# Kernel optimization log

Hardware: AMD Instinct MI355X
Metric: run time of the kernel (lower is better)

Reference implementation:

```python
import jax, jax.numpy as jnp
import numpy as np

H, D, K = 8, 64, 9           # new num heads, head size, conv kernel size
A = H * D                    # all_head_size = 512
HID = 2 * A                  # input hidden size = 1024
STD = 0.02


def setup_inputs() -> dict:
    key = jax.random.key(0)
    ks = jax.random.split(key, 16)
    B, S = 4, 2048
    f = jnp.float32
    inp = {
        'hidden_states': jax.random.normal(ks[0], (B, S, HID), f),
        'Wq': jax.random.normal(ks[1], (A, A), f) * STD,
        'bq': jnp.zeros((A,), f),
        'Wk': jax.random.normal(ks[2], (A, A), f) * STD,
        'bk': jnp.zeros((A,), f),
        'Wv': jax.random.normal(ks[3], (A, A), f) * STD,
        'bv': jnp.zeros((A,), f),
        'dw_w': jax.random.normal(ks[4], (A, 1, K), f) * STD,   # depthwise conv (groups=A)
        'pw_w': jax.random.normal(ks[5], (A, A, 1), f) * STD,   # pointwise 1x1 conv
        'sep_b': jnp.zeros((A, 1), f),                          # SeparableConv1D bias
        'Wck': jax.random.normal(ks[6], (H * K, A), f) * STD,   # conv_kernel_layer
        'bck': jnp.zeros((H * K,), f),
        'Wco': jax.random.normal(ks[7], (A, A), f) * STD,       # conv_out_layer
        'bco': jnp.zeros((A,), f),
    }
    return inp


def reference(hidden_states, Wq, bq, Wk, bk, Wv, bv, dw_w, pw_w, sep_b, Wck, bck, Wco, bco):
    B, S, _ = hidden_states.shape
    hs_attn = hidden_states[:, :, :A]
    hs_conv = hidden_states[:, :, A:]

    q = hs_attn @ Wq.T + bq
    k = hs_attn @ Wk.T + bk
    v = hs_attn @ Wv.T + bv

    # SeparableConv1D on (B, A, S): depthwise then pointwise, plus bias
    x = hs_conv.transpose(0, 2, 1)
    x = jax.lax.conv_general_dilated(
        x, dw_w, window_strides=(1,), padding=[(K // 2, K // 2)],
        feature_group_count=A, dimension_numbers=('NCH', 'OIH', 'NCH'))
    x = jnp.einsum('bcs,oc->bos', x, pw_w[:, :, 0]) + sep_b
    mixed_key_conv = x.transpose(0, 2, 1)            # (B,S,A)

    # per-token softmax conv kernel
    conv_attn = mixed_key_conv * hs_conv
    ckl = (conv_attn @ Wck.T + bck).reshape(B, S, H, K)
    ckl = jax.nn.softmax(ckl, axis=-1)               # softmax over kernel taps

    # dynamic-span lightweight convolution (unfold -> batched matmul)
    col = hs_conv @ Wco.T + bco                      # (B,S,A)
    pad = jnp.pad(col, ((0, 0), (K // 2, K // 2), (0, 0)))
    windows = jnp.stack([pad[:, i:i + S] for i in range(K)], axis=-1)  # (B,S,A,K)
    windows = windows.reshape(B, S, H, D, K)
    conv_out = jnp.einsum('bshdk,bshk->bshd', windows, ckl)            # (B,S,H,D)

    # standard self-attention
    qh = q.reshape(B, S, H, D).transpose(0, 2, 1, 3)
    kh = k.reshape(B, S, H, D).transpose(0, 2, 1, 3)
    vh = v.reshape(B, S, H, D).transpose(0, 2, 1, 3)
    scale = jnp.asarray(1.0 / np.sqrt(D), q.dtype)
    scores = jnp.einsum('bhqd,bhkd->bhqk', qh, kh) * scale
    probs = jax.nn.softmax(scores, axis=-1)
    ctx = jnp.einsum('bhqk,bhkd->bqhd', probs, vh)   # (B,S,H,D)

    out = jnp.concatenate([ctx, conv_out], axis=2)   # (B,S,2H,D)
    return out.reshape(B, S, HID)
```

## Files before the change

kernel.cpp:

```cpp
#include <hip/hip_runtime.h>
#include <hip/hip_bf16.h>

#define NH   8
#define HD   64
#define KW   9
#define AD   512
#define HIDD 1024
#define BB   4
#define SS   2048
#define MTOK (BB*SS)
#define WSZ  262144

typedef __attribute__((ext_vector_type(8))) short short8;
typedef __attribute__((ext_vector_type(4))) float floatx4;
typedef __attribute__((ext_vector_type(16))) float floatx16;

__device__ __forceinline__ short f2bf(float f) {
    unsigned u = __float_as_uint(f);
    u = (u + 0x7FFFu + ((u >> 16) & 1u)) >> 16;
    return (short)u;
}
__device__ __forceinline__ float bf2f(short s) {
    return __uint_as_float(((unsigned)(unsigned short)s) << 16);
}
__device__ __forceinline__ float exp2_raw(float x) {
    return __builtin_amdgcn_exp2f(x);
}
__device__ __forceinline__ unsigned pkbf2(float a, float b) {
    unsigned au = __float_as_uint(a) + 0x8000u;
    unsigned bu = __float_as_uint(b) + 0x8000u;
    return __builtin_amdgcn_perm(bu, au, 0x07060302);
}
__device__ __forceinline__ void gl2lds16(const short* g, short* l) {
    __builtin_amdgcn_global_load_lds(
        (const __attribute__((address_space(1))) void*)g,
        (__attribute__((address_space(3))) void*)l, 16, 0, 0);
}

__global__ __launch_bounds__(256) void cvt_hs_kernel(
    const float* __restrict__ hs, short* __restrict__ hsb)
{
    int idx = blockIdx.x * 256 + threadIdx.x;
    const float* s = hs + (long)idx * 8;
    float4 a = *(const float4*)s, c = *(const float4*)(s + 4);
    short8 o;
    o[0]=f2bf(a.x); o[1]=f2bf(a.y); o[2]=f2bf(a.z); o[3]=f2bf(a.w);
    o[4]=f2bf(c.x); o[5]=f2bf(c.y); o[6]=f2bf(c.z); o[7]=f2bf(c.w);
    *(short8*)(hsb + (long)idx * 8) = o;
}

__global__ __launch_bounds__(256) void cvt_w_kernel(
    const float* __restrict__ pw, const float* __restrict__ Wco,
    const float* __restrict__ Wq, const float* __restrict__ Wk,
    const float* __restrict__ Wv, const float* __restrict__ Wck,
    const float* __restrict__ dw,
    short* __restrict__ dst, float* __restrict__ dwT)
{
    int idx = blockIdx.x * 256 + threadIdx.x;
    if (idx >= 172032) {
        int t = idx - 172032;
        if (t < AD * KW) {
            int c = t / KW, k = t - c * KW;
            dwT[k * AD + c] = dw[t];
        }
        return;
    }
    int e0 = idx * 8;
    short8 o;
    if (e0 < 5 * WSZ) {
        int w = e0 >> 18, off = e0 & (WSZ - 1);
        const float* src = (w == 0) ? pw : (w == 1) ? Wco : (w == 2) ? Wq
                         : (w == 3) ? Wk : Wv;
        float4 a = *(const float4*)(src + off), c = *(const float4*)(src + off + 4);
        o[0]=f2bf(a.x); o[1]=f2bf(a.y); o[2]=f2bf(a.z); o[3]=f2bf(a.w);
        o[4]=f2bf(c.x); o[5]=f2bf(c.y); o[6]=f2bf(c.z); o[7]=f2bf(c.w);
    } else {
        int off = e0 - 5 * WSZ;
        int row = off >> 9, col = off & 511;
        if (row < NH * KW) {
            const float* src = Wck + row * AD + col;
            float4 a = *(const float4*)src, c = *(const float4*)(src + 4);
            o[0]=f2bf(a.x); o[1]=f2bf(a.y); o[2]=f2bf(a.z); o[3]=f2bf(a.w);
            o[4]=f2bf(c.x); o[5]=f2bf(c.y); o[6]=f2bf(c.z); o[7]=f2bf(c.w);
        } else {
            for (int i = 0; i < 8; ++i) o[i] = 0;
        }
    }
    *(short8*)(dst + e0) = o;
}

__global__ __launch_bounds__(256) void dwconv_kernel(
    const short* __restrict__ hsb, const float* __restrict__ dwT,
    short* __restrict__ x1)
{
    int idx = blockIdx.x * 256 + threadIdx.x;
    int c8  = (idx & 63) * 8;
    int tok = idx >> 6;
    int s   = tok & (SS - 1);
    int b   = tok >> 11;
    const short* base = hsb + (long)(b * SS) * HIDD + AD + c8;
    float acc[8];
#pragma unroll
    for (int i = 0; i < 8; ++i) acc[i] = 0.f;
#pragma unroll
    for (int kk = 0; kk < KW; ++kk) {
        int ss2 = s + kk - KW / 2;
        if (ss2 >= 0 && ss2 < SS) {
            short8 hv = *(const short8*)(base + (long)ss2 * HIDD);
            float4 w0 = *(const float4*)(dwT + kk * AD + c8);
            float4 w1 = *(const float4*)(dwT + kk * AD + c8 + 4);
            acc[0] += w0.x * bf2f(hv[0]); acc[1] += w0.y * bf2f(hv[1]);
            acc[2] += w0.z * bf2f(hv[2]); acc[3] += w0.w * bf2f(hv[3]);
            acc[4] += w1.x * bf2f(hv[4]); acc[5] += w1.y * bf2f(hv[5]);
            acc[6] += w1.z * bf2f(hv[6]); acc[7] += w1.w * bf2f(hv[7]);
        }
    }
    short8 o;
#pragma unroll
    for (int i = 0; i < 8; ++i) o[i] = f2bf(acc[i]);
    *(short8*)(x1 + (long)tok * AD + c8) = o;
}

template<int FM, int FN, int MODE>
__global__ __launch_bounds__(256) void gemm_bf16_kernel(
    const short* __restrict__ X, int ldx, int xoff,
    const short* __restrict__ W,
    const float* __restrict__ b0p, const float* __restrict__ b1p,
    const float* __restrict__ b2p,
    const short* __restrict__ mulp, int mul_ld, int mul_off,
    void* __restrict__ Cout, short* __restrict__ vtout,
    int ldc, int N, int Kd, float oscale)
{
    constexpr int TM = 32 * FM, TN = 32 * FN;
    __shared__ __align__(16) short As[TM * 64];
    __shared__ __align__(16) short Bs[TN * 64];
    const int tid  = threadIdx.x;
    const int wv   = tid >> 6, lane = tid & 63;
    const int ln   = lane & 15, quad = lane >> 4;
    const int wm   = wv >> 1, wn = wv & 1;
    const int m0 = blockIdx.x * TM, n0 = blockIdx.y * TN;

    floatx4 acc[FM][FN];
#pragma unroll
    for (int i = 0; i < FM; ++i)
#pragma unroll
        for (int j = 0; j < FN; ++j) acc[i][j] = (floatx4){0.f, 0.f, 0.f, 0.f};

    const short* xbase = X + (long)m0 * ldx + xoff;
    const short* wbase = W + (long)n0 * Kd;

    for (int k0 = 0; k0 < Kd; k0 += 64) {
#pragma unroll
        for (int g = tid; g < TM * 8; g += 256) {
            int m = g >> 3, p = g & 7, gk = p ^ (m & 7);
            gl2lds16(xbase + (long)m * ldx + k0 + gk * 8, &As[g * 8]);
        }
#pragma unroll
        for (int g = tid; g < TN * 8; g += 256) {
            int m = g >> 3, p = g & 7, gk = p ^ (m & 7);
            gl2lds16(wbase + (long)m * Kd + k0 + gk * 8, &Bs[g * 8]);
        }
        __syncthreads();
#pragma unroll
        for (int half = 0; half < 2; ++half) {
            short8 afr[FM], bfr[FN];
#pragma unroll
            for (int i = 0; i < FM; ++i) {
                int p = (half * 4 + quad) ^ (ln & 7);
                afr[i] = *(const short8*)&As[(wm * 16 * FM + i * 16 + ln) * 64 + p * 8];
            }
#pragma unroll
            for (int j = 0; j < FN; ++j) {
                int p = (half * 4 + quad) ^ (ln & 7);
                bfr[j] = *(const short8*)&Bs[(wn * 16 * FN + j * 16 + ln) * 64 + p * 8];
            }
#pragma unroll
            for (int i = 0; i < FM; ++i)
#pragma unroll
                for (int j = 0; j < FN; ++j)
                    acc[i][j] = __builtin_amdgcn_mfma_f32_16x16x32_bf16(
                        afr[i], bfr[j], acc[i][j], 0, 0, 0);
        }
        __syncthreads();
    }

#pragma unroll
    for (int j = 0; j < FN; ++j) {
        int n = n0 + wn * 16 * FN + j * 16 + ln;
        if constexpr (MODE == 3) {
            if (n >= 1024) {
                int hh = (n - 1024) >> 6, dd = (n - 1024) & 63;
                float bv = b2p[n - 1024];
                int mblk = m0 + wm * 16 * FM;
                int bidx = mblk >> 11, sblk = mblk & (SS - 1);
                short* dst = vtout + ((long)((bidx * NH + hh) * HD + dd)) * SS + sblk;
#pragma unroll
                for (int i = 0; i < FM; ++i) {
                    unsigned lo = pkbf2(acc[i][j][0] + bv, acc[i][j][1] + bv);
                    unsigned hi = pkbf2(acc[i][j][2] + bv, acc[i][j][3] + bv);
                    *(uint2*)(dst + i * 16 + quad * 4) = make_uint2(lo, hi);
                }
            } else {
                float bv = (n < 512) ? b0p[n] : b1p[n - 512];
                float sc = (n < 512) ? oscale : 1.f;
#pragma unroll
                for (int i = 0; i < FM; ++i) {
#pragma unroll
                    for (int r = 0; r < 4; ++r) {
                        int m = m0 + wm * 16 * FM + i * 16 + quad * 4 + r;
                        float val = (acc[i][j][r] + bv) * sc;
                        ((short*)Cout)[(long)m * ldc + n] = f2bf(val);
                    }
                }
            }
        } else if (n < N) {
            float bv = b0p[n], sc = oscale;
#pragma unroll
            for (int i = 0; i < FM; ++i) {
#pragma unroll
                for (int r = 0; r < 4; ++r) {
                    int m = m0 + wm * 16 * FM + i * 16 + quad * 4 + r;
                    float val = (acc[i][j][r] + bv) * sc;
                    if constexpr (MODE == 2)
                        val *= bf2f(mulp[(long)m * mul_ld + mul_off + n]);
                    if constexpr (MODE == 0)
                        ((float*)Cout)[(long)m * ldc + n] = val;
                    else
                        ((short*)Cout)[(long)m * ldc + n] = f2bf(val);
                }
            }
        }
    }
}

__global__ __launch_bounds__(256) void convout_kernel(
    const short* __restrict__ col, const float* __restrict__ ckl,
    float* __restrict__ out)
{
    int idx = blockIdx.x * 256 + threadIdx.x;
    int d4  = (idx & 127) * 4;
    int tok = idx >> 7;
    int s   = tok & (SS - 1);
    int b   = tok >> 11;
    int h   = d4 >> 6;
    const float* lg = ckl + (long)tok * (NH * KW) + h * KW;
    float wv[KW];
    float mx = -1e30f;
#pragma unroll
    for (int i = 0; i < KW; ++i) { wv[i] = lg[i]; mx = fmaxf(mx, wv[i]); }
    float sum = 0.f;
#pragma unroll
    for (int i = 0; i < KW; ++i) { wv[i] = __expf(wv[i] - mx); sum += wv[i]; }
    float inv = 1.f / sum;
    float a0 = 0.f, a1 = 0.f, a2 = 0.f, a3 = 0.f;
    const short* cbase = col + (long)(b * SS) * AD + d4;
#pragma unroll
    for (int kk = 0; kk < KW; ++kk) {
        int ss2 = s + kk - KW / 2;
        if (ss2 >= 0 && ss2 < SS) {
            uint2 cv = *(const uint2*)(cbase + (long)ss2 * AD);
            float w = wv[kk];
            a0 += w * bf2f((short)(cv.x & 0xFFFF));
            a1 += w * bf2f((short)(cv.x >> 16));
            a2 += w * bf2f((short)(cv.y & 0xFFFF));
            a3 += w * bf2f((short)(cv.y >> 16));
        }
    }
    *(float4*)&out[(long)tok * HIDD + AD + d4] =
        make_float4(a0 * inv, a1 * inv, a2 * inv, a3 * inv);
}

__global__ __launch_bounds__(256) void flash_mfma_kernel(
    const short* __restrict__ qkv, const short* __restrict__ vT,
    float* __restrict__ out)
{
    const int qt = blockIdx.x, h = blockIdx.y, b = blockIdx.z;
    const int tid  = threadIdx.x;
    const int w    = tid >> 6;
    const int lane = tid & 63;
    const int l5   = lane & 31;
    const int hh   = lane >> 5;

    __shared__ __align__(16) short Kb[64 * 64];
    __shared__ __align__(16) short Vt[64 * 64];
    __shared__ float ls[4][32];

    const int  q0 = qt * 128 + w * 32;
    const long rowbase = (long)b * SS;

    short8 qf[4];
    {
        const short* qrow = qkv + (rowbase + q0 + l5) * 1536 + h * HD;
#pragma unroll
        for (int i = 0; i < 4; ++i)
            qf[i] = *(const short8*)(qrow + i * 16 + hh * 8);
    }

    floatx16 acc0, acc1;
#pragma unroll
    for (int r = 0; r < 16; ++r) { acc0[r] = 0.f; acc1[r] = 0.f; }
    float l_i = 0.f;

    const int m1 = tid >> 3,  gk1 = (tid & 7) ^ (m1 & 7);
    const int g2 = 256 + tid;
    const int m2 = g2 >> 3,   gk2 = (g2 & 7) ^ (m2 & 7);
    const short* kbase  = qkv + 512 + rowbase * 1536 + h * HD;
    const short* vtbase = vT + ((long)(b * NH + h) * HD) * SS;
    const short* sk0 = kbase  + (long)m1 * 1536 + gk1 * 8;
    const short* sk1 = kbase  + (long)m2 * 1536 + gk2 * 8;
    const short* sv0 = vtbase + (long)m1 * SS   + gk1 * 8;
    const short* sv1 = vtbase + (long)m2 * SS   + gk2 * 8;
    short* const dk0 = &Kb[tid * 8];
    short* const dk1 = &Kb[g2 * 8];
    short* const dv0 = &Vt[tid * 8];
    short* const dv1 = &Vt[g2 * 8];

#define STAGE_K() do { gl2lds16(sk0, dk0); gl2lds16(sk1, dk1); \
                       sk0 += 64 * 1536; sk1 += 64 * 1536; } while (0)
#define STAGE_V() do { gl2lds16(sv0, dv0); gl2lds16(sv1, dv1); \
                       sv0 += 64; sv1 += 64; } while (0)

    auto qkt_pack = [&](short8* pf) {
        floatx16 S0, S1;
#pragma unroll
        for (int r = 0; r < 16; ++r) { S0[r] = 0.f; S1[r] = 0.f; }
#pragma unroll
        for (int i = 0; i < 4; ++i) {
            int p = (2 * i + hh) ^ (l5 & 7);
            short8 k0 = *(const short8*)&Kb[l5 * 64 + p * 8];
            short8 k1 = *(const short8*)&Kb[(32 + l5) * 64 + p * 8];
            S0 = __builtin_amdgcn_mfma_f32_32x32x16_bf16(k0, qf[i], S0, 0, 0, 0);
            S1 = __builtin_amdgcn_mfma_f32_32x32x16_bf16(k1, qf[i], S1, 0, 0, 0);
        }
        float pe0[16], pe1[16];
#pragma unroll
        for (int r = 0; r < 16; ++r) {
            pe0[r] = exp2_raw(S0[r]);
            pe1[r] = exp2_raw(S1[r]);
        }
        float s = 0.f;
#pragma unroll
        for (int r = 0; r < 16; ++r) s += pe0[r] + pe1[r];
        l_i += s;
#pragma unroll
        for (int t = 0; t < 2; ++t) {
            const float* pe = t ? pe1 : pe0;
#pragma unroll
            for (int u = 0; u < 2; ++u) {
                unsigned a0 = pkbf2(pe[8 * u + 0], pe[8 * u + 1]);
                unsigned a1 = pkbf2(pe[8 * u + 2], pe[8 * u + 3]);
                unsigned b0 = pkbf2(pe[8 * u + 4], pe[8 * u + 5]);
                unsigned b1 = pkbf2(pe[8 * u + 6], pe[8 * u + 7]);
                asm("v_permlane32_swap_b32 %0, %1" : "+v"(a0), "+v"(b0));
                asm("v_permlane32_swap_b32 %0, %1" : "+v"(a1), "+v"(b1));
                union { uint4 u4; short8 s8; } cv;
                cv.u4 = make_uint4(a0, a1, b0, b1);
                pf[t * 2 + u] = cv.s8;
            }
        }
    };

    auto pv_phase = [&](const short8* pf) {
#pragma unroll
        for (int s = 0; s < 4; ++s) {
            int p = (2 * s + hh) ^ (l5 & 7);
            short8 v0 = *(const short8*)&Vt[l5 * 64 + p * 8];
            short8 v1 = *(const short8*)&Vt[(32 + l5) * 64 + p * 8];
            acc0 = __builtin_amdgcn_mfma_f32_32x32x16_bf16(pf[s], v0, acc0, 0, 0, 0);
            acc1 = __builtin_amdgcn_mfma_f32_32x32x16_bf16(pf[s], v1, acc1, 0, 0, 0);
        }
    };

    STAGE_K();
    STAGE_V();
    asm volatile("s_waitcnt vmcnt(0)" ::: "memory");
    __builtin_amdgcn_s_barrier();
    asm volatile("" ::: "memory");

    const int NT = SS / 64;
    short8 pf[4];
    for (int kt = 0; kt < NT - 1; ++kt) {
        qkt_pack(pf);
        __builtin_amdgcn_s_barrier();
        asm volatile("" ::: "memory");
        STAGE_K();
        asm volatile("s_waitcnt vmcnt(2)" ::: "memory");
        __builtin_amdgcn_s_barrier();
        asm volatile("" ::: "memory");
        pv_phase(pf);
        __builtin_amdgcn_s_barrier();
        asm volatile("" ::: "memory");
        STAGE_V();
        asm volatile("s_waitcnt vmcnt(2)" ::: "memory");
        __builtin_amdgcn_s_barrier();
        asm volatile("" ::: "memory");
    }
    qkt_pack(pf);
    asm volatile("s_waitcnt vmcnt(0)" ::: "memory");
    __builtin_amdgcn_s_barrier();
    asm volatile("" ::: "memory");
    pv_phase(pf);

#undef STAGE_K
#undef STAGE_V

    l_i += __shfl_xor(l_i, 32);
    ls[w][l5] = 1.f / l_i;
    float4 lv[4];
#pragma unroll
    for (int g = 0; g < 4; ++g)
        lv[g] = *(const float4*)&ls[w][8 * g + 4 * hh];

#pragma unroll
    for (int r = 0; r < 16; ++r) {
        int g = r >> 2, j = r & 3;
        int qr = j + 8 * g + 4 * hh;
        float iv = lv[g][j];
        float* orow = out + (rowbase + q0 + qr) * HIDD + h * HD;
        orow[l5]      = acc0[r] * iv;
        orow[32 + l5] = acc1[r] * iv;
    }
}

extern "C" void kernel_launch(void* const* d_in, const int* in_sizes, int n_in,
                              void* d_out, int out_size, void* d_ws, size_t ws_size,
                              hipStream_t stream)
{
    const float* hs   = (const float*)d_in[0];
    const float* Wq   = (const float*)d_in[1];
    const float* bq   = (const float*)d_in[2];
    const float* Wk   = (const float*)d_in[3];
    const float* bk   = (const float*)d_in[4];
    const float* Wv   = (const float*)d_in[5];
    const float* bv   = (const float*)d_in[6];
    const float* dw   = (const float*)d_in[7];
    const float* pw   = (const float*)d_in[8];
    const float* sepb = (const float*)d_in[9];
    const float* Wck  = (const float*)d_in[10];
    const float* bck  = (const float*)d_in[11];
    const float* Wco  = (const float*)d_in[12];
    const float* bco  = (const float*)d_in[13];
    float* out = (float*)d_out;

    short* hsb  = (short*)d_ws;
    short* x1c  = hsb + (long)MTOK * HIDD;
    short* qkvb = x1c + (long)MTOK * AD;
    short* vTb  = qkvb + (long)MTOK * 1536;
    float* ckl  = (float*)(vTb + (long)MTOK * AD);
    short* wb   = (short*)(ckl + (long)MTOK * (NH * KW));
    short* pw_b   = wb;
    short* Wco_b  = wb + 1L * WSZ;
    short* Wqkv_b = wb + 2L * WSZ;
    short* Wck_b  = wb + 5L * WSZ;
    float* dwT    = (float*)(Wck_b + 128L * AD);
    short* cab    = qkvb;

    const float QSCALE = 0.18033688011112042f;

    cvt_hs_kernel<<<MTOK * HIDD / 2048, 256, 0, stream>>>(hs, hsb);
    cvt_w_kernel<<<690, 256, 0, stream>>>(
        pw, Wco, Wq, Wk, Wv, Wck, dw, wb, dwT);
    dwconv_kernel<<<MTOK * AD / 2048, 256, 0, stream>>>(hsb, dwT, x1c);
    gemm_bf16_kernel<2, 2, 2><<<dim3(MTOK / 64, AD / 64), 256, 0, stream>>>(
        x1c, AD, 0, pw_b, sepb, nullptr, nullptr, hsb, HIDD, AD,
        cab, nullptr, AD, AD, AD, 1.f);
    gemm_bf16_kernel<2, 2, 0><<<dim3(MTOK / 64, 2), 256, 0, stream>>>(
        cab, AD, 0, Wck_b, bck, nullptr, nullptr, nullptr, 0, 0,
        ckl, nullptr, NH * KW, NH * KW, AD, 1.f);
    gemm_bf16_kernel<2, 2, 1><<<dim3(MTOK / 64, AD / 64), 256, 0, stream>>>(
        hsb, HIDD, AD, Wco_b, bco, nullptr, nullptr, nullptr, 0, 0,
        x1c, nullptr, AD, AD, AD, 1.f);
    convout_kernel<<<MTOK * AD / 1024, 256, 0, stream>>>(x1c, ckl, out);
    gemm_bf16_kernel<4, 4, 3><<<dim3(MTOK / 128, 1536 / 128), 256, 0, stream>>>(
        hsb, HIDD, 0, Wqkv_b, bq, bk, bv, nullptr, 0, 0,
        qkvb, vTb, 1536, 1536, AD, QSCALE);
    flash_mfma_kernel<<<dim3(SS / 128, NH, BB), 256, 0, stream>>>(qkvb, vTb, out);

    (void)in_sizes; (void)n_in; (void)out_size; (void)ws_size;
}
```

Baseline: 232.9 us.

## Split flash attention keys across wave pairs and merge partial results in LDS

The flash attention kernel now uses 64 queries per block, with two wave pairs each handling alternate 64-key tiles. Their partial accumulators and row sums are reduced through shared memory at the end, and the grid doubles to 1024 blocks, giving more parallelism across CUs. It also packs bf16 with the hardware v_cvt_pk_bf16_f32 instruction, raises MFMA wave priority with s_setprio, and sets a launch-bounds occupancy hint. The exchange is an extra LDS reduction step, more total staging traffic for Q, and possible register pressure from the occupancy hint.

```diff
diff --git a/kernel.cpp b/kernel.cpp
--- a/kernel.cpp
+++ b/kernel.cpp
@@ -27,9 +27,9 @@
     return __builtin_amdgcn_exp2f(x);
 }
 __device__ __forceinline__ unsigned pkbf2(float a, float b) {
-    unsigned au = __float_as_uint(a) + 0x8000u;
-    unsigned bu = __float_as_uint(b) + 0x8000u;
-    return __builtin_amdgcn_perm(bu, au, 0x07060302);
+    unsigned d;
+    asm("v_cvt_pk_bf16_f32 %0, %1, %2" : "=v"(d) : "v"(a), "v"(b));
+    return d;
 }
 __device__ __forceinline__ void gl2lds16(const short* g, short* l) {
     __builtin_amdgcn_global_load_lds(
@@ -270,7 +270,7 @@
         make_float4(a0 * inv, a1 * inv, a2 * inv, a3 * inv);
 }
 
-__global__ __launch_bounds__(256) void flash_mfma_kernel(
+__global__ __launch_bounds__(256, 4) void flash_mfma_kernel(
     const short* __restrict__ qkv, const short* __restrict__ vT,
     float* __restrict__ out)
 {
@@ -280,12 +280,18 @@
     const int lane = tid & 63;
     const int l5   = lane & 31;
     const int hh   = lane >> 5;
-
-    __shared__ __align__(16) short Kb[64 * 64];
-    __shared__ __align__(16) short Vt[64 * 64];
-    __shared__ float ls[4][32];
-
-    const int  q0 = qt * 128 + w * 32;
+    const int qhalf = w & 1;
+    const int kpar  = w >> 1;
+    const int ptid  = tid & 127;
+
+    __shared__ __align__(16) short smem[4][4096];
+    __shared__ float ls[2][32];
+    float* const cbuf = (float*)smem;
+
+    short* const Kb = smem[kpar];
+    short* const Vt = smem[2 + kpar];
+
+    const int  q0 = qt * 64 + qhalf * 32;
     const long rowbase = (long)b * SS;
 
     short8 qf[4];
@@ -301,29 +307,44 @@
     for (int r = 0; r < 16; ++r) { acc0[r] = 0.f; acc1[r] = 0.f; }
     float l_i = 0.f;
 
-    const int m1 = tid >> 3,  gk1 = (tid & 7) ^ (m1 & 7);
-    const int g2 = 256 + tid;
-    const int m2 = g2 >> 3,   gk2 = (g2 & 7) ^ (m2 & 7);
-    const short* kbase  = qkv + 512 + rowbase * 1536 + h * HD;
-    const short* vtbase = vT + ((long)(b * NH + h) * HD) * SS;
-    const short* sk0 = kbase  + (long)m1 * 1536 + gk1 * 8;
-    const short* sk1 = kbase  + (long)m2 * 1536 + gk2 * 8;
-    const short* sv0 = vtbase + (long)m1 * SS   + gk1 * 8;
-    const short* sv1 = vtbase + (long)m2 * SS   + gk2 * 8;
-    short* const dk0 = &Kb[tid * 8];
-    short* const dk1 = &Kb[g2 * 8];
-    short* const dv0 = &Vt[tid * 8];
-    short* const dv1 = &Vt[g2 * 8];
-
-#define STAGE_K() do { gl2lds16(sk0, dk0); gl2lds16(sk1, dk1); \
-                       sk0 += 64 * 1536; sk1 += 64 * 1536; } while (0)
-#define STAGE_V() do { gl2lds16(sv0, dv0); gl2lds16(sv1, dv1); \
-                       sv0 += 64; sv1 += 64; } while (0)
+    const short* kb_s[4];
+    const short* vt_s[4];
+    short* kb_d[4];
+    short* vt_d[4];
+    {
+        const short* kbase  = qkv + 512 + rowbase * 1536 + h * HD
+                            + (long)kpar * 64 * 1536;
+        const short* vtbase = vT + ((long)(b * NH + h) * HD) * SS + kpar * 64;
+#pragma unroll
+        for (int j = 0; j < 4; ++j) {
+            int g = ptid + 128 * j, m = g >> 3, p = g & 7, gk = p ^ (m & 7);
+            kb_s[j] = kbase + (long)m * 1536 + gk * 8;
+            vt_s[j] = vtbase + (long)m * SS + gk * 8;
+            kb_d[j] = &Kb[g * 8];
+            vt_d[j] = &Vt[g * 8];
+        }
+    }
+
+    auto STAGE_K = [&]() {
+#pragma unroll
+        for (int j = 0; j < 4; ++j) {
+            gl2lds16(kb_s[j], kb_d[j]);
+            kb_s[j] += 128 * 1536;
+        }
+    };
+    auto STAGE_V = [&]() {
+#pragma unroll
+        for (int j = 0; j < 4; ++j) {
+            gl2lds16(vt_s[j], vt_d[j]);
+            vt_s[j] += 128;
+        }
+    };
 
     auto qkt_pack = [&](short8* pf) {
         floatx16 S0, S1;
 #pragma unroll
         for (int r = 0; r < 16; ++r) { S0[r] = 0.f; S1[r] = 0.f; }
+        __builtin_amdgcn_s_setprio(1);
 #pragma unroll
         for (int i = 0; i < 4; ++i) {
             int p = (2 * i + hh) ^ (l5 & 7);
@@ -332,6 +353,7 @@
             S0 = __builtin_amdgcn_mfma_f32_32x32x16_bf16(k0, qf[i], S0, 0, 0, 0);
             S1 = __builtin_amdgcn_mfma_f32_32x32x16_bf16(k1, qf[i], S1, 0, 0, 0);
         }
+        __builtin_amdgcn_s_setprio(0);
         float pe0[16], pe1[16];
 #pragma unroll
         for (int r = 0; r < 16; ++r) {
@@ -361,6 +383,7 @@
     };
 
     auto pv_phase = [&](const short8* pf) {
+        __builtin_amdgcn_s_setprio(1);
 #pragma unroll
         for (int s = 0; s < 4; ++s) {
             int p = (2 * s + hh) ^ (l5 & 7);
@@ -369,6 +392,7 @@
             acc0 = __builtin_amdgcn_mfma_f32_32x32x16_bf16(pf[s], v0, acc0, 0, 0, 0);
             acc1 = __builtin_amdgcn_mfma_f32_32x32x16_bf16(pf[s], v1, acc1, 0, 0, 0);
         }
+        __builtin_amdgcn_s_setprio(0);
     };
 
     STAGE_K();
@@ -377,21 +401,21 @@
     __builtin_amdgcn_s_barrier();
     asm volatile("" ::: "memory");
 
-    const int NT = SS / 64;
+    const int NT2 = SS / 128;
     short8 pf[4];
-    for (int kt = 0; kt < NT - 1; ++kt) {
+    for (int t = 0; t < NT2 - 1; ++t) {
         qkt_pack(pf);
         __builtin_amdgcn_s_barrier();
         asm volatile("" ::: "memory");
         STAGE_K();
-        asm volatile("s_waitcnt vmcnt(2)" ::: "memory");
+        asm volatile("s_waitcnt vmcnt(4)" ::: "memory");
         __builtin_amdgcn_s_barrier();
         asm volatile("" ::: "memory");
         pv_phase(pf);
         __builtin_amdgcn_s_barrier();
         asm volatile("" ::: "memory");
         STAGE_V();
-        asm volatile("s_waitcnt vmcnt(2)" ::: "memory");
+        asm volatile("s_waitcnt vmcnt(4)" ::: "memory");
         __builtin_amdgcn_s_barrier();
         asm volatile("" ::: "memory");
     }
@@ -401,24 +425,53 @@
     asm volatile("" ::: "memory");
     pv_phase(pf);
 
-#undef STAGE_K
-#undef STAGE_V
-
-    l_i += __shfl_xor(l_i, 32);
-    ls[w][l5] = 1.f / l_i;
-    float4 lv[4];
-#pragma unroll
-    for (int g = 0; g < 4; ++g)
-        lv[g] = *(const float4*)&ls[w][8 * g + 4 * hh];
-
-#pragma unroll
-    for (int r = 0; r < 16; ++r) {
-        int g = r >> 2, j = r & 3;
-        int qr = j + 8 * g + 4 * hh;
-        float iv = lv[g][j];
-        float* orow = out + (rowbase + q0 + qr) * HIDD + h * HD;
-        orow[l5]      = acc0[r] * iv;
-        orow[32 + l5] = acc1[r] * iv;
+    __builtin_amdgcn_s_barrier();
+    asm volatile("" ::: "memory");
+    if (w >= 2) {
+        float* dst = cbuf + ((w - 2) * 64 + lane) * 36;
+#pragma unroll
+        for (int k = 0; k < 4; ++k)
+            *(float4*)(dst + 4 * k) =
+                make_float4(acc0[4*k], acc0[4*k+1], acc0[4*k+2], acc0[4*k+3]);
+#pragma unroll
+        for (int k = 0; k < 4; ++k)
+            *(float4*)(dst + 16 + 4 * k) =
+                make_float4(acc1[4*k], acc1[4*k+1], acc1[4*k+2], acc1[4*k+3]);
+        dst[32] = l_i;
+    }
+    __builtin_amdgcn_s_barrier();
+    asm volatile("" ::: "memory");
+    if (w < 2) {
+        const float* src = cbuf + (w * 64 + lane) * 36;
+#pragma unroll
+        for (int k = 0; k < 4; ++k) {
+            float4 v = *(const float4*)(src + 4 * k);
+            acc0[4*k] += v.x; acc0[4*k+1] += v.y;
+            acc0[4*k+2] += v.z; acc0[4*k+3] += v.w;
+        }
+#pragma unroll
+        for (int k = 0; k < 4; ++k) {
+            float4 v = *(const float4*)(src + 16 + 4 * k);
+            acc1[4*k] += v.x; acc1[4*k+1] += v.y;
+            acc1[4*k+2] += v.z; acc1[4*k+3] += v.w;
+        }
+        l_i += src[32];
+        l_i += __shfl_xor(l_i, 32);
+        ls[w][l5] = 1.f / l_i;
+        float4 lv[4];
+#pragma unroll
+        for (int g = 0; g < 4; ++g)
+            lv[g] = *(const float4*)&ls[w][8 * g + 4 * hh];
+
+#pragma unroll
+        for (int r = 0; r < 16; ++r) {
+            int g = r >> 2, j = r & 3;
+            int qr = j + 8 * g + 4 * hh;
+            float iv = lv[g][j];
+            float* orow = out + (rowbase + q0 + qr) * HIDD + h * HD;
+            orow[l5]      = acc0[r] * iv;
+            orow[32 + l5] = acc1[r] * iv;
+        }
     }
 }
 
@@ -474,7 +527,7 @@
     gemm_bf16_kernel<4, 4, 3><<<dim3(MTOK / 128, 1536 / 128), 256, 0, stream>>>(
         hsb, HIDD, 0, Wqkv_b, bq, bk, bv, nullptr, 0, 0,
         qkvb, vTb, 1536, 1536, AD, QSCALE);
-    flash_mfma_kernel<<<dim3(SS / 128, NH, BB), 256, 0, stream>>>(qkvb, vTb, out);
+    flash_mfma_kernel<<<dim3(SS / 64, NH, BB), 256, 0, stream>>>(qkvb, vTb, out);
 
     (void)in_sizes; (void)n_in; (void)out_size; (void)ws_size;
 }
```

Result: slower. 246.7 us (+5.9%).

## Double-buffer K/V tiles and software-pipeline QK^T with PV in flash kernel

Applied to the files above, without the earlier changes.

Restructures the flash attention loop to double-buffer K and V tiles in LDS and interleave the QK^T of tile t+1 with the PV of tile t. This cuts the barriers per iteration from four to one and lets loads overlap compute. It also raises wave priority around the MFMA sections, seeds the first MFMA from a zero register, and uses a native bf16 pack instruction for probabilities. In exchange it doubles LDS use for K/V and keeps two sets of probability fragments live, which may lower occupancy or increase register pressure.

```diff
diff --git a/kernel.cpp b/kernel.cpp
--- a/kernel.cpp
+++ b/kernel.cpp
@@ -27,9 +27,9 @@
     return __builtin_amdgcn_exp2f(x);
 }
 __device__ __forceinline__ unsigned pkbf2(float a, float b) {
-    unsigned au = __float_as_uint(a) + 0x8000u;
-    unsigned bu = __float_as_uint(b) + 0x8000u;
-    return __builtin_amdgcn_perm(bu, au, 0x07060302);
+    unsigned d;
+    asm("v_cvt_pk_bf16_f32 %0, %1, %2" : "=v"(d) : "v"(a), "v"(b));
+    return d;
 }
 __device__ __forceinline__ void gl2lds16(const short* g, short* l) {
     __builtin_amdgcn_global_load_lds(
@@ -281,8 +281,8 @@
     const int l5   = lane & 31;
     const int hh   = lane >> 5;
 
-    __shared__ __align__(16) short Kb[64 * 64];
-    __shared__ __align__(16) short Vt[64 * 64];
+    __shared__ __align__(16) short Kb[2][64 * 64];
+    __shared__ __align__(16) short Vb[2][64 * 64];
     __shared__ float ls[4][32];
 
     const int  q0 = qt * 128 + w * 32;
@@ -297,8 +297,9 @@
     }
 
     floatx16 acc0, acc1;
-#pragma unroll
-    for (int r = 0; r < 16; ++r) { acc0[r] = 0.f; acc1[r] = 0.f; }
+    floatx16 Z;
+#pragma unroll
+    for (int r = 0; r < 16; ++r) { acc0[r] = 0.f; acc1[r] = 0.f; Z[r] = 0.f; }
     float l_i = 0.f;
 
     const int m1 = tid >> 3,  gk1 = (tid & 7) ^ (m1 & 7);
@@ -310,28 +311,37 @@
     const short* sk1 = kbase  + (long)m2 * 1536 + gk2 * 8;
     const short* sv0 = vtbase + (long)m1 * SS   + gk1 * 8;
     const short* sv1 = vtbase + (long)m2 * SS   + gk2 * 8;
-    short* const dk0 = &Kb[tid * 8];
-    short* const dk1 = &Kb[g2 * 8];
-    short* const dv0 = &Vt[tid * 8];
-    short* const dv1 = &Vt[g2 * 8];
-
-#define STAGE_K() do { gl2lds16(sk0, dk0); gl2lds16(sk1, dk1); \
-                       sk0 += 64 * 1536; sk1 += 64 * 1536; } while (0)
-#define STAGE_V() do { gl2lds16(sv0, dv0); gl2lds16(sv1, dv1); \
-                       sv0 += 64; sv1 += 64; } while (0)
-
-    auto qkt_pack = [&](short8* pf) {
-        floatx16 S0, S1;
-#pragma unroll
-        for (int r = 0; r < 16; ++r) { S0[r] = 0.f; S1[r] = 0.f; }
-#pragma unroll
-        for (int i = 0; i < 4; ++i) {
+
+    auto STAGE_K = [&](int buf) {
+        gl2lds16(sk0, &Kb[buf][tid * 8]);
+        gl2lds16(sk1, &Kb[buf][g2 * 8]);
+        sk0 += 64 * 1536; sk1 += 64 * 1536;
+    };
+    auto STAGE_V = [&](int buf) {
+        gl2lds16(sv0, &Vb[buf][tid * 8]);
+        gl2lds16(sv1, &Vb[buf][g2 * 8]);
+        sv0 += 64; sv1 += 64;
+    };
+
+    auto qkt = [&](const short* KB, floatx16& S0, floatx16& S1) {
+        {
+            int p = hh ^ (l5 & 7);
+            short8 k0 = *(const short8*)&KB[l5 * 64 + p * 8];
+            short8 k1 = *(const short8*)&KB[(32 + l5) * 64 + p * 8];
+            S0 = __builtin_amdgcn_mfma_f32_32x32x16_bf16(k0, qf[0], Z, 0, 0, 0);
+            S1 = __builtin_amdgcn_mfma_f32_32x32x16_bf16(k1, qf[0], Z, 0, 0, 0);
+        }
+#pragma unroll
+        for (int i = 1; i < 4; ++i) {
             int p = (2 * i + hh) ^ (l5 & 7);
-            short8 k0 = *(const short8*)&Kb[l5 * 64 + p * 8];
-            short8 k1 = *(const short8*)&Kb[(32 + l5) * 64 + p * 8];
+            short8 k0 = *(const short8*)&KB[l5 * 64 + p * 8];
+            short8 k1 = *(const short8*)&KB[(32 + l5) * 64 + p * 8];
             S0 = __builtin_amdgcn_mfma_f32_32x32x16_bf16(k0, qf[i], S0, 0, 0, 0);
             S1 = __builtin_amdgcn_mfma_f32_32x32x16_bf16(k1, qf[i], S1, 0, 0, 0);
         }
+    };
+
+    auto smax = [&](const floatx16& S0, const floatx16& S1, short8* pf) {
         float pe0[16], pe1[16];
 #pragma unroll
         for (int r = 0; r < 16; ++r) {
@@ -360,49 +370,76 @@
         }
     };
 
-    auto pv_phase = [&](const short8* pf) {
+    auto pv = [&](const short* VB, const short8* pf) {
 #pragma unroll
         for (int s = 0; s < 4; ++s) {
             int p = (2 * s + hh) ^ (l5 & 7);
-            short8 v0 = *(const short8*)&Vt[l5 * 64 + p * 8];
-            short8 v1 = *(const short8*)&Vt[(32 + l5) * 64 + p * 8];
+            short8 v0 = *(const short8*)&VB[l5 * 64 + p * 8];
+            short8 v1 = *(const short8*)&VB[(32 + l5) * 64 + p * 8];
             acc0 = __builtin_amdgcn_mfma_f32_32x32x16_bf16(pf[s], v0, acc0, 0, 0, 0);
             acc1 = __builtin_amdgcn_mfma_f32_32x32x16_bf16(pf[s], v1, acc1, 0, 0, 0);
         }
     };
 
-    STAGE_K();
-    STAGE_V();
+    const int NT = SS / 64;
+    short8 pfA[4], pfB[4];
+
+    STAGE_K(0);
     asm volatile("s_waitcnt vmcnt(0)" ::: "memory");
     __builtin_amdgcn_s_barrier();
     asm volatile("" ::: "memory");
 
-    const int NT = SS / 64;
-    short8 pf[4];
-    for (int kt = 0; kt < NT - 1; ++kt) {
-        qkt_pack(pf);
+    {
+        STAGE_K(1); STAGE_V(0);
+        floatx16 S0, S1;
+        qkt(Kb[0], S0, S1);
+        smax(S0, S1, pfA);
+        asm volatile("s_waitcnt vmcnt(0)" ::: "memory");
         __builtin_amdgcn_s_barrier();
         asm volatile("" ::: "memory");
-        STAGE_K();
-        asm volatile("s_waitcnt vmcnt(2)" ::: "memory");
+    }
+
+    for (int t = 1; t + 1 < NT; t += 2) {
+        {
+            STAGE_K(0); STAGE_V(1);
+            floatx16 S0, S1;
+            __builtin_amdgcn_s_setprio(1);
+            qkt(Kb[1], S0, S1);
+            pv(Vb[0], pfA);
+            __builtin_amdgcn_s_setprio(0);
+            smax(S0, S1, pfB);
+            asm volatile("s_waitcnt vmcnt(0)" ::: "memory");
+            __builtin_amdgcn_s_barrier();
+            asm volatile("" ::: "memory");
+        }
+        {
+            if (t + 2 < NT) STAGE_K(1);
+            STAGE_V(0);
+            floatx16 S0, S1;
+            __builtin_amdgcn_s_setprio(1);
+            qkt(Kb[0], S0, S1);
+            pv(Vb[1], pfB);
+            __builtin_amdgcn_s_setprio(0);
+            smax(S0, S1, pfA);
+            asm volatile("s_waitcnt vmcnt(0)" ::: "memory");
+            __builtin_amdgcn_s_barrier();
+            asm volatile("" ::: "memory");
+        }
+    }
+
+    {
+        STAGE_V(1);
+        floatx16 S0, S1;
+        __builtin_amdgcn_s_setprio(1);
+        qkt(Kb[1], S0, S1);
+        pv(Vb[0], pfA);
+        __builtin_amdgcn_s_setprio(0);
+        smax(S0, S1, pfB);
+        asm volatile("s_waitcnt vmcnt(0)" ::: "memory");
         __builtin_amdgcn_s_barrier();
         asm volatile("" ::: "memory");
-        pv_phase(pf);
-        __builtin_amdgcn_s_barrier();
-        asm volatile("" ::: "memory");
-        STAGE_V();
-        asm volatile("s_waitcnt vmcnt(2)" ::: "memory");
-        __builtin_amdgcn_s_barrier();
-        asm volatile("" ::: "memory");
-    }
-    qkt_pack(pf);
-    asm volatile("s_waitcnt vmcnt(0)" ::: "memory");
-    __builtin_amdgcn_s_barrier();
-    asm volatile("" ::: "memory");
-    pv_phase(pf);
-
-#undef STAGE_K
-#undef STAGE_V
+    }
+    pv(Vb[1], pfB);
 
     l_i += __shfl_xor(l_i, 32);
     ls[w][l5] = 1.f / l_i;
```

Result: no change. 229.9 us (-1.3%).
